# Optimization experiments

Hardware: AMD Instinct MI355X
Metric: run time of the kernel (lower is better)

The kernel has to match this reference:

```python
import jax, jax.numpy as jnp
import numpy as np

# Dims (match init_kwargs): d_model=1024, H=16 heads, hd=64, lift=2 -> Nlift=128, top-k t=32
B, T, D = 1, 2048, 1024
H, HD, LIFT, TK = 16, 64, 2, 32
N = LIFT * HD  # 128 lifted dims per head
EPS = 1e-12


def topk_sparsify(x, k):
    """ReLU then keep only the top-k values per last-dim row (rest zeroed).
    Mathematically identical to the torch COO top-k construction: the sparse
    matrix equals the dense matrix with non-top-k entries zeroed."""
    x = jax.nn.relu(x)
    vals, idx = jax.lax.top_k(x, k)              # (..., k)
    n = x.shape[-1]
    flat_idx = idx.reshape(-1, k)
    flat_vals = vals.reshape(-1, k)
    R = flat_idx.shape[0]
    out = jnp.zeros((R, n), dtype=x.dtype)
    out = out.at[jnp.arange(R)[:, None], flat_idx].set(flat_vals)
    return out.reshape(x.shape)


def setup_inputs() -> dict:
    key = jax.random.key(0)
    ks = jax.random.split(key, 6)
    x = jax.random.normal(ks[0], (B, T, D), jnp.float32)
    W_q = jax.random.normal(ks[1], (H * N, D), jnp.float32) * 0.02
    W_k = jax.random.normal(ks[2], (H * N, D), jnp.float32) * 0.02
    W_v = jax.random.normal(ks[3], (H * HD, D), jnp.float32) * 0.02
    W_o = jax.random.normal(ks[4], (D, H * HD), jnp.float32) * 0.02
    sink = jax.random.normal(ks[5], (H, HD), jnp.float32) * 0.02
    log_beta = jnp.zeros((), jnp.float32)
    return {"x": x, "W_q": W_q, "W_k": W_k, "W_v": W_v, "W_o": W_o,
            "sink": sink, "log_beta": log_beta}


def reference(x, W_q, W_k, W_v, W_o, sink, log_beta):
    # Projections (Linear with no bias: x @ W.T)
    q = (x @ W_q.T).reshape(B, T, H, N)
    k = (x @ W_k.T).reshape(B, T, H, N)
    v = (x @ W_v.T).reshape(B, T, H, HD)

    # ReLU + top-k sparsification of lifted Q/K rows
    qs = topk_sparsify(q, TK).transpose(0, 2, 1, 3)  # (B,H,T,N)
    kk = topk_sparsify(k, TK).transpose(0, 2, 1, 3)  # (B,H,T,N)

    # A = Qs @ Ks^T per (batch, head) block; spspmm only produces same-block
    # entries, so the per-head batched matmul is the exact dense equivalent.
    A = jnp.einsum('bhin,bhjn->bhij', qs, kk)        # (B,H,T,T), all >= 0

    # Causal filter: keep j <= i
    causal = jnp.tril(jnp.ones((T, T), dtype=bool))
    A = jnp.where(causal, A, jnp.zeros((), A.dtype))

    # p=1 normalization with learned sink mass beta
    denom = A.sum(-1)                                # (B,H,T)
    beta = jnp.exp(log_beta)
    denom_ws = denom + beta
    A = A / jnp.maximum(denom_ws, EPS)[..., None]

    vh = v.transpose(0, 2, 1, 3)                     # (B,H,T,HD)
    Y = jnp.einsum('bhij,bhjd->bhid', A, vh)         # (B,H,T,HD)
    Y = Y + (beta / denom_ws)[..., None] * sink[None, :, None, :]

    Y = Y.transpose(0, 2, 1, 3).reshape(B, T, H * HD)
    return Y @ W_o.T
```

## Files before the change

### kernel.cpp

```cpp
#include <hip/hip_runtime.h>

typedef __attribute__((ext_vector_type(8))) short bf8v;
typedef __attribute__((ext_vector_type(4))) float f4v;
typedef unsigned short u16;
typedef unsigned int   u32;
#define AS1 __attribute__((address_space(1)))
#define AS3 __attribute__((address_space(3)))

__device__ inline u16 f2b(float f){
  u32 u = __builtin_bit_cast(u32, f);
  u += 0x7fffu + ((u >> 16) & 1u);
  return (u16)(u >> 16);
}

__global__ __launch_bounds__(256) void conv_all(const float* __restrict__ x,  const float* __restrict__ wq,
                                                const float* __restrict__ wk, const float* __restrict__ wv,
                                                const float* __restrict__ wo,
                                                u16* xb, u16* wqb, u16* wkb, u16* wvb, u16* wob){
  int i = blockIdx.x * 256 + threadIdx.x;
  const float* src; u16* dst; int off;
  if      (i <  524288){ src = x;  dst = xb;  off = i; }
  else if (i < 1048576){ src = wq; dst = wqb; off = i -  524288; }
  else if (i < 1572864){ src = wk; dst = wkb; off = i - 1048576; }
  else if (i < 1835008){ src = wv; dst = wvb; off = i - 1572864; }
  else                 { src = wo; dst = wob; off = i - 1835008; }
  float4 v = ((const float4*)src)[off];
  uint2 r;
  r.x = (u32)f2b(v.x) | ((u32)f2b(v.y) << 16);
  r.y = (u32)f2b(v.z) | ((u32)f2b(v.w) << 16);
  ((uint2*)dst)[off] = r;
}

__device__ __forceinline__ void gemm_core(const u16* __restrict__ A, const u16* __restrict__ B,
                                          int K, int m0, int n0, u16* lds, f4v acc[4][4]){
  const int tid = threadIdx.x;
  const int l = tid & 63, w = tid >> 6;
  const int wrow = (w >> 1) * 64, wcol = (w & 1) * 64;
  #pragma unroll
  for (int a = 0; a < 4; a++)
    #pragma unroll
    for (int b = 0; b < 4; b++) acc[a][b] = (f4v)0.0f;

  const int crow = l >> 3;
  const int ksrc = ((l & 7) ^ crow) * 8;

  auto stage = [&](int k0, int buf){
    const u16* Abase = A + (size_t)m0 * K + k0;
    const u16* Bbase = B + (size_t)n0 * K + k0;
    u16* At = lds + buf * 16384;
    u16* Bt = At + 8192;
    #pragma unroll
    for (int c = 0; c < 4; c++){
      int chunk = w * 4 + c;
      int row = chunk * 8 + crow;
      __builtin_amdgcn_global_load_lds((const AS1 void*)(Abase + (size_t)row * K + ksrc),
                                       (AS3 void*)(At + chunk * 512), 16, 0, 0);
      __builtin_amdgcn_global_load_lds((const AS1 void*)(Bbase + (size_t)row * K + ksrc),
                                       (AS3 void*)(Bt + chunk * 512), 16, 0, 0);
    }
  };

  stage(0, 0);
  __syncthreads();
  int buf = 0;
  for (int k0 = 0; k0 < K; k0 += 64){
    if (k0 + 64 < K) stage(k0 + 64, buf ^ 1);
    const u16* At = lds + buf * 16384;
    const u16* Bt = At + 8192;
    #pragma unroll
    for (int kk = 0; kk < 2; kk++){
      bf8v af[4], bfr[4];
      #pragma unroll
      for (int mr = 0; mr < 4; mr++){
        int row = wrow + mr * 16 + (l & 15);
        af[mr] = *(const bf8v*)(At + row * 64 + (((kk * 32 + (l >> 4) * 8)) ^ ((row & 7) * 8)));
      }
      #pragma unroll
      for (int nc = 0; nc < 4; nc++){
        int row = wcol + nc * 16 + (l & 15);
        bfr[nc] = *(const bf8v*)(Bt + row * 64 + (((kk * 32 + (l >> 4) * 8)) ^ ((row & 7) * 8)));
      }
      #pragma unroll
      for (int mr = 0; mr < 4; mr++)
        #pragma unroll
        for (int nc = 0; nc < 4; nc++)
          acc[mr][nc] = __builtin_amdgcn_mfma_f32_16x16x32_bf16(af[mr], bfr[nc], acc[mr][nc], 0, 0, 0);
    }
    __syncthreads();
    buf ^= 1;
  }
}

__global__ __launch_bounds__(256) void qkv_gemm(const u16* __restrict__ xb,
                                                const u16* __restrict__ wqb, const u16* __restrict__ wkb,
                                                const u16* __restrict__ wvb,
                                                float* qf, float* kf, u16* vtb){
  __shared__ u16 lds[32768];
  int b = (blockIdx.x & 7) * 80 + (blockIdx.x >> 3);
  const u16* Bp; int which;
  if (b < 256)      { Bp = wqb; which = 0; }
  else if (b < 512) { Bp = wkb; which = 1; b -= 256; }
  else              { Bp = wvb; which = 2; b -= 512; }
  int sh = (which == 2) ? 3 : 4;
  int m0 = (b >> sh) * 128, n0 = (b & ((1 << sh) - 1)) * 128;

  f4v acc[4][4];
  gemm_core(xb, Bp, 1024, m0, n0, lds, acc);

  const int l = threadIdx.x & 63, w = threadIdx.x >> 6;
  const int wrow = (w >> 1) * 64, wcol = (w & 1) * 64;
  if (which < 2){
    float* C = which ? kf : qf;
    #pragma unroll
    for (int mr = 0; mr < 4; mr++)
      #pragma unroll
      for (int nc = 0; nc < 4; nc++)
        #pragma unroll
        for (int rr = 0; rr < 4; rr++){
          int row = m0 + wrow + mr * 16 + (l >> 4) * 4 + rr;
          int col = n0 + wcol + nc * 16 + (l & 15);
          C[(size_t)row * 2048 + col] = acc[mr][nc][rr];
        }
  } else {
    #pragma unroll
    for (int mr = 0; mr < 4; mr++)
      #pragma unroll
      for (int nc = 0; nc < 4; nc++){
        int gcol = n0 + wcol + nc * 16 + (l & 15);
        int t0 = m0 + wrow + mr * 16 + (l >> 4) * 4;
        uint2 pk;
        pk.x = (u32)f2b(acc[mr][nc][0]) | ((u32)f2b(acc[mr][nc][1]) << 16);
        pk.y = (u32)f2b(acc[mr][nc][2]) | ((u32)f2b(acc[mr][nc][3]) << 16);
        *(uint2*)(vtb + (size_t)gcol * 2048 + t0) = pk;
      }
  }
}

__global__ __launch_bounds__(256) void o_gemm(const u16* __restrict__ yb, const u16* __restrict__ wob,
                                              float* out){
  __shared__ u16 lds[32768];
  int b = (blockIdx.x & 7) * 16 + (blockIdx.x >> 3);
  int m0 = (b >> 3) * 128, n0 = (b & 7) * 128;
  f4v acc[4][4];
  gemm_core(yb, wob, 1024, m0, n0, lds, acc);
  const int l = threadIdx.x & 63, w = threadIdx.x >> 6;
  const int wrow = (w >> 1) * 64, wcol = (w & 1) * 64;
  #pragma unroll
  for (int mr = 0; mr < 4; mr++)
    #pragma unroll
    for (int nc = 0; nc < 4; nc++)
      #pragma unroll
      for (int rr = 0; rr < 4; rr++){
        int row = m0 + wrow + mr * 16 + (l >> 4) * 4 + rr;
        int col = n0 + wcol + nc * 16 + (l & 15);
        out[(size_t)row * 1024 + col] = acc[mr][nc][rr];
      }
}

__global__ __launch_bounds__(256) void topk2(const float* __restrict__ qf, const float* __restrict__ kf,
                                             u16* __restrict__ qsb, u16* __restrict__ ksb){
  int w = threadIdx.x >> 6, l = threadIdx.x & 63;
  int b = blockIdx.x;
  const float* src; u16* dst;
  if (b < 8192){ src = qf; dst = qsb; } else { src = kf; dst = ksb; b -= 8192; }
  int row = b * 4 + w;
  int t = row >> 4, h = row & 15;
  const float* sp = src + (size_t)t * 2048 + h * 128 + l * 2;
  float v0 = sp[0], v1 = sp[1];
  v0 = v0 > 0.f ? v0 : 0.f;
  v1 = v1 > 0.f ? v1 : 0.f;
  u32 u0 = __builtin_bit_cast(u32, v0), u1 = __builtin_bit_cast(u32, v1);
  u32 pre = 0;
  for (int bb = 30; bb >= 0; --bb){
    u32 cand = pre | (1u << bb);
    int c = __builtin_popcountll(__ballot(u0 >= cand)) + __builtin_popcountll(__ballot(u1 >= cand));
    if (c >= 32) pre = cand;
  }
  u16 o0 = (u0 >= pre) ? f2b(v0) : (u16)0;
  u16 o1 = (u1 >= pre) ? f2b(v1) : (u16)0;
  ((u32*)(dst + ((size_t)h * 2048 + t) * 128))[l] = (u32)o0 | ((u32)o1 << 16);
}

__global__ __launch_bounds__(512) void attn3(const u16* __restrict__ qs, const u16* __restrict__ ks,
                                             const u16* __restrict__ vt, const float* __restrict__ sink,
                                             const float* __restrict__ logbeta, u16* __restrict__ yout,
                                             float* __restrict__ Yp, float* __restrict__ Dp){
  __shared__ u16 Kt[2][8192];
  __shared__ u16 Vt[2][4096];
  __shared__ u16 St[8][16 * 72];
  const int tid = threadIdx.x, l = tid & 63, w = tid >> 6;
  const int b = blockIdx.x;
  const int slot = b >> 3;
  const int h = (b & 7) + 8 * (slot / 40);
  const int u = slot % 40;
  int it, chunk, nch;
  if (u < 4)       { it = u; chunk = 0; nch = 1; }
  else if (u < 12) { it = 4 + ((u - 4) >> 1);  chunk = (u - 4) & 1;  nch = 2; }
  else if (u < 24) { it = 8 + (u - 12) / 3;    chunk = (u - 12) % 3; nch = 3; }
  else             { it = 12 + ((u - 24) >> 2); chunk = (u - 24) & 3; nch = 4; }
  const int jt0 = chunk * 8;
  const int jt1 = min(jt0 + 8, 2 * it + 2);
  const int qrow0 = it * 128 + w * 16;
  const float beta = expf(logbeta[0]);

  bf8v qfr[4];
  {
    int trow = qrow0 + (l & 15);
    const u16* qrow = qs + ((size_t)h * 2048 + trow) * 128 + (l >> 4) * 8;
    #pragma unroll
    for (int kk = 0; kk < 4; kk++) qfr[kk] = *(const bf8v*)(qrow + kk * 32);
  }

  f4v accY[4];
  #pragma unroll
  for (int c = 0; c < 4; c++) accY[c] = (f4v)0.0f;
  float dsum[4] = {0.f, 0.f, 0.f, 0.f};

  const u16* kroot = ks + (size_t)h * 2048 * 128;
  const u16* vroot = vt + (size_t)h * 64 * 2048;

  auto stage = [&](int jt, int buf){
    const u16* kbase = kroot + (size_t)jt * 64 * 128;
    #pragma unroll
    for (int i = 0; i < 2; i++){
      int g = i * 512 + tid;
      int r = g >> 4, c = g & 15;
      __builtin_amdgcn_global_load_lds((const AS1 void*)(kbase + r * 128 + (c ^ (r & 7)) * 8),
                                       (AS3 void*)(&Kt[buf][(i * 512 + w * 64) * 8]), 16, 0, 0);
    }
    {
      int d = tid >> 3, c = tid & 7;
      __builtin_amdgcn_global_load_lds((const AS1 void*)(vroot + (size_t)d * 2048 + jt * 64 + (c ^ (d & 7)) * 8),
                                       (AS3 void*)(&Vt[buf][w * 512]), 16, 0, 0);
    }
  };

  stage(jt0, 0);
  __syncthreads();
  int buf = 0;
  for (int jt = jt0; jt < jt1; ++jt){
    if (jt + 1 < jt1) stage(jt + 1, buf ^ 1);

    if (jt * 64 <= qrow0 + 15){
      f4v accS[4];
      #pragma unroll
      for (int c = 0; c < 4; c++) accS[c] = (f4v)0.0f;
      __builtin_amdgcn_s_setprio(1);
      #pragma unroll
      for (int c = 0; c < 4; c++){
        int r = c * 16 + (l & 15);
        #pragma unroll
        for (int kk = 0; kk < 4; kk++){
          int ch = kk * 4 + (l >> 4);
          bf8v kfr = *(const bf8v*)(&Kt[buf][r * 128 + ((ch ^ (r & 7)) * 8)]);
          accS[c] = __builtin_amdgcn_mfma_f32_16x16x32_bf16(qfr[kk], kfr, accS[c], 0, 0, 0);
        }
      }
      __builtin_amdgcn_s_setprio(0);
      if (jt * 64 + 63 > qrow0){
        #pragma unroll
        for (int c = 0; c < 4; c++)
          #pragma unroll
          for (int rr = 0; rr < 4; rr++){
            int i = qrow0 + (l >> 4) * 4 + rr;
            int j = jt * 64 + c * 16 + (l & 15);
            if (j > i) accS[c][rr] = 0.f;
          }
      }
      #pragma unroll
      for (int c = 0; c < 4; c++)
        #pragma unroll
        for (int rr = 0; rr < 4; rr++){
          dsum[rr] += accS[c][rr];
          St[w][((l >> 4) * 4 + rr) * 72 + c * 16 + (l & 15)] = f2b(accS[c][rr]);
        }
      __builtin_amdgcn_s_setprio(1);
      #pragma unroll
      for (int k2 = 0; k2 < 2; k2++){
        bf8v afr = *(const bf8v*)(&St[w][(l & 15) * 72 + k2 * 32 + (l >> 4) * 8]);
        #pragma unroll
        for (int c = 0; c < 4; c++){
          int d = c * 16 + (l & 15);
          int ch = k2 * 4 + (l >> 4);
          bf8v vfr = *(const bf8v*)(&Vt[buf][d * 64 + ((ch ^ (d & 7)) * 8)]);
          accY[c] = __builtin_amdgcn_mfma_f32_16x16x32_bf16(afr, vfr, accY[c], 0, 0, 0);
        }
      }
      __builtin_amdgcn_s_setprio(0);
    }
    __syncthreads();
    buf ^= 1;
  }

  #pragma unroll
  for (int rr = 0; rr < 4; rr++){
    float s = dsum[rr];
    s += __shfl_xor(s, 1, 64);
    s += __shfl_xor(s, 2, 64);
    s += __shfl_xor(s, 4, 64);
    s += __shfl_xor(s, 8, 64);
    dsum[rr] = s;
  }

  if (nch == 1){
    #pragma unroll
    for (int c = 0; c < 4; c++){
      float sv = sink[h * 64 + c * 16 + (l & 15)];
      #pragma unroll
      for (int rr = 0; rr < 4; rr++){
        float den = dsum[rr] + beta;
        float inv = 1.0f / fmaxf(den, 1e-12f);
        float y = (accY[c][rr] + beta * sv) * inv;
        int row = qrow0 + (l >> 4) * 4 + rr;
        yout[(size_t)row * 1024 + h * 64 + c * 16 + (l & 15)] = f2b(y);
      }
    }
  } else {
    float* yp = Yp + ((size_t)h * 40 + u) * 8192;
    #pragma unroll
    for (int c = 0; c < 4; c++)
      #pragma unroll
      for (int rr = 0; rr < 4; rr++){
        int rowib = w * 16 + (l >> 4) * 4 + rr;
        yp[rowib * 64 + c * 16 + (l & 15)] = accY[c][rr];
      }
    if ((l & 15) == 0){
      #pragma unroll
      for (int rr = 0; rr < 4; rr++)
        Dp[((size_t)h * 40 + u) * 128 + w * 16 + (l >> 4) * 4 + rr] = dsum[rr];
    }
  }
}

__global__ __launch_bounds__(256) void attn_reduce(const float* __restrict__ Yp, const float* __restrict__ Dp,
                                                   const float* __restrict__ sink, const float* __restrict__ logbeta,
                                                   u16* __restrict__ yout){
  int blk = blockIdx.x;
  int h = blk / 12, it = 4 + blk % 12;
  int nch = it / 4 + 1;
  int u0 = (it < 8) ? 4 + (it - 4) * 2 : (it < 12) ? 12 + (it - 8) * 3 : 24 + (it - 12) * 4;
  float beta = expf(logbeta[0]);
  __shared__ float inv_s[128];
  int t = threadIdx.x;
  if (t < 128){
    float s = 0.f;
    for (int c = 0; c < nch; c++) s += Dp[((size_t)h * 40 + u0 + c) * 128 + t];
    inv_s[t] = 1.0f / fmaxf(s + beta, 1e-12f);
  }
  __syncthreads();
  const float* base = Yp + ((size_t)h * 40 + u0) * 8192;
  #pragma unroll
  for (int e = 0; e < 32; e++){
    int idx = e * 256 + t;
    float acc = 0.f;
    for (int c = 0; c < nch; c++) acc += base[c * 8192 + idx];
    int row = idx >> 6, col = idx & 63;
    float y = (acc + beta * sink[h * 64 + col]) * inv_s[row];
    yout[(size_t)(it * 128 + row) * 1024 + h * 64 + col] = f2b(y);
  }
}

extern "C" void kernel_launch(void* const* d_in, const int* in_sizes, int n_in,
                              void* d_out, int out_size, void* d_ws, size_t ws_size,
                              hipStream_t stream){
  const float* x    = (const float*)d_in[0];
  const float* Wq   = (const float*)d_in[1];
  const float* Wk   = (const float*)d_in[2];
  const float* Wv   = (const float*)d_in[3];
  const float* Wo   = (const float*)d_in[4];
  const float* sink = (const float*)d_in[5];
  const float* logb = (const float*)d_in[6];

  char* ws = (char*)d_ws;
  u16*   xb  = (u16*)(ws + 0);
  u16*   wqb = (u16*)(ws + 4194304);
  u16*   wkb = (u16*)(ws + 8388608);
  u16*   wvb = (u16*)(ws + 12582912);
  u16*   wob = (u16*)(ws + 14680064);
  float* qf  = (float*)(ws + 16777216);
  float* kf  = (float*)(ws + 33554432);
  u16*   qsb = (u16*)(ws + 50331648);
  u16*   ksb = (u16*)(ws + 58720256);
  u16*   vtb = (u16*)(ws + 67108864);
  u16*   yb  = (u16*)(ws + 71303168);
  float* Yp  = (float*)(ws + 16777216);
  float* Dp  = (float*)(ws + 37748736);

  conv_all<<<8192, 256, 0, stream>>>(x, Wq, Wk, Wv, Wo, xb, wqb, wkb, wvb, wob);
  qkv_gemm<<<640, 256, 0, stream>>>(xb, wqb, wkb, wvb, qf, kf, vtb);
  topk2<<<16384, 256, 0, stream>>>(qf, kf, qsb, ksb);
  attn3<<<640, 512, 0, stream>>>(qsb, ksb, vtb, sink, logb, yb, Yp, Dp);
  attn_reduce<<<192, 256, 0, stream>>>(Yp, Dp, sink, logb, yb);
  o_gemm<<<128, 256, 0, stream>>>(yb, wob, (float*)d_out);
}
```

Baseline: 151.5 us.

## Deepen GEMM pipeline to five-stage K32 ring and store Q/K projections as bf16

The shared GEMM core moves from a double-buffered K=64 tile loop to a five-slot ring of K=32 tiles with three stages in flight. It uses explicit vmcnt waits, a raw s_barrier and raised priority around the MFMA block, so global-to-LDS loads overlap more with compute. Separately, the QKV GEMM writes Q and K as bf16 instead of fp32, and the top-k kernel selects directly on the bf16 bits with a 15-bit radix search. This halves the projection write and read traffic. Top-k ties are now resolved at bf16 precision rather than fp32, which can change which entries are kept.

```diff
diff --git a/kernel.cpp b/kernel.cpp
--- a/kernel.cpp
+++ b/kernel.cpp
@@ -41,61 +41,71 @@
     #pragma unroll
     for (int b = 0; b < 4; b++) acc[a][b] = (f4v)0.0f;
 
-  const int crow = l >> 3;
-  const int ksrc = ((l & 7) ^ crow) * 8;
-
-  auto stage = [&](int k0, int buf){
-    const u16* Abase = A + (size_t)m0 * K + k0;
-    const u16* Bbase = B + (size_t)n0 * K + k0;
-    u16* At = lds + buf * 16384;
-    u16* Bt = At + 8192;
-    #pragma unroll
-    for (int c = 0; c < 4; c++){
-      int chunk = w * 4 + c;
-      int row = chunk * 8 + crow;
-      __builtin_amdgcn_global_load_lds((const AS1 void*)(Abase + (size_t)row * K + ksrc),
-                                       (AS3 void*)(At + chunk * 512), 16, 0, 0);
-      __builtin_amdgcn_global_load_lds((const AS1 void*)(Bbase + (size_t)row * K + ksrc),
-                                       (AS3 void*)(Bt + chunk * 512), 16, 0, 0);
-    }
+  const int c0 = w * 64 + l;
+  const int c1 = c0 + 256;
+  const int r0 = c0 >> 2, s0e = ((c0 & 3) ^ ((r0 >> 1) & 3)) * 8;
+  const int r1 = c1 >> 2, s1e = ((c1 & 3) ^ ((r1 >> 1) & 3)) * 8;
+
+  const u16* Aroot = A + (size_t)m0 * K;
+  const u16* Broot = B + (size_t)n0 * K;
+
+  auto stage = [&](int k0, int bb){
+    const u16* Ab = Aroot + k0;
+    const u16* Bb = Broot + k0;
+    __builtin_amdgcn_global_load_lds((const AS1 void*)(Ab + (size_t)r0 * K + s0e),
+                                     (AS3 void*)(lds + bb + w * 512), 16, 0, 0);
+    __builtin_amdgcn_global_load_lds((const AS1 void*)(Ab + (size_t)r1 * K + s1e),
+                                     (AS3 void*)(lds + bb + 2048 + w * 512), 16, 0, 0);
+    __builtin_amdgcn_global_load_lds((const AS1 void*)(Bb + (size_t)r0 * K + s0e),
+                                     (AS3 void*)(lds + bb + 4096 + w * 512), 16, 0, 0);
+    __builtin_amdgcn_global_load_lds((const AS1 void*)(Bb + (size_t)r1 * K + s1e),
+                                     (AS3 void*)(lds + bb + 6144 + w * 512), 16, 0, 0);
   };
 
+  const int nst = K >> 5;
   stage(0, 0);
-  __syncthreads();
-  int buf = 0;
-  for (int k0 = 0; k0 < K; k0 += 64){
-    if (k0 + 64 < K) stage(k0 + 64, buf ^ 1);
-    const u16* At = lds + buf * 16384;
-    const u16* Bt = At + 8192;
-    #pragma unroll
-    for (int kk = 0; kk < 2; kk++){
-      bf8v af[4], bfr[4];
-      #pragma unroll
-      for (int mr = 0; mr < 4; mr++){
-        int row = wrow + mr * 16 + (l & 15);
-        af[mr] = *(const bf8v*)(At + row * 64 + (((kk * 32 + (l >> 4) * 8)) ^ ((row & 7) * 8)));
-      }
-      #pragma unroll
-      for (int nc = 0; nc < 4; nc++){
-        int row = wcol + nc * 16 + (l & 15);
-        bfr[nc] = *(const bf8v*)(Bt + row * 64 + (((kk * 32 + (l >> 4) * 8)) ^ ((row & 7) * 8)));
-      }
-      #pragma unroll
-      for (int mr = 0; mr < 4; mr++)
-        #pragma unroll
-        for (int nc = 0; nc < 4; nc++)
-          acc[mr][nc] = __builtin_amdgcn_mfma_f32_16x16x32_bf16(af[mr], bfr[nc], acc[mr][nc], 0, 0, 0);
-    }
-    __syncthreads();
-    buf ^= 1;
+  stage(32, 8192);
+  stage(64, 16384);
+
+  const int kb = l >> 4;
+  for (int i = 0; i < nst; ++i){
+    int k3 = (i + 3) << 5;
+    if (k3 < K) stage(k3, ((i + 3) % 5) * 8192);
+    if      (i <  nst - 3) asm volatile("s_waitcnt vmcnt(12)" ::: "memory");
+    else if (i == nst - 3) asm volatile("s_waitcnt vmcnt(8)"  ::: "memory");
+    else if (i == nst - 2) asm volatile("s_waitcnt vmcnt(4)"  ::: "memory");
+    else                   asm volatile("s_waitcnt vmcnt(0)"  ::: "memory");
+    __builtin_amdgcn_sched_barrier(0);
+    __builtin_amdgcn_s_barrier();
+
+    const u16* At = lds + (i % 5) * 8192;
+    const u16* Bt = At + 4096;
+    bf8v af[4], bfr[4];
+    #pragma unroll
+    for (int mr = 0; mr < 4; mr++){
+      int row = wrow + mr * 16 + (l & 15);
+      af[mr] = *(const bf8v*)(At + row * 32 + ((kb ^ ((row >> 1) & 3)) * 8));
+    }
+    #pragma unroll
+    for (int nc = 0; nc < 4; nc++){
+      int row = wcol + nc * 16 + (l & 15);
+      bfr[nc] = *(const bf8v*)(Bt + row * 32 + ((kb ^ ((row >> 1) & 3)) * 8));
+    }
+    __builtin_amdgcn_s_setprio(1);
+    #pragma unroll
+    for (int mr = 0; mr < 4; mr++)
+      #pragma unroll
+      for (int nc = 0; nc < 4; nc++)
+        acc[mr][nc] = __builtin_amdgcn_mfma_f32_16x16x32_bf16(af[mr], bfr[nc], acc[mr][nc], 0, 0, 0);
+    __builtin_amdgcn_s_setprio(0);
   }
 }
 
 __global__ __launch_bounds__(256) void qkv_gemm(const u16* __restrict__ xb,
                                                 const u16* __restrict__ wqb, const u16* __restrict__ wkb,
                                                 const u16* __restrict__ wvb,
-                                                float* qf, float* kf, u16* vtb){
-  __shared__ u16 lds[32768];
+                                                u16* qf, u16* kf, u16* vtb){
+  __shared__ u16 lds[40960];
   int b = (blockIdx.x & 7) * 80 + (blockIdx.x >> 3);
   const u16* Bp; int which;
   if (b < 256)      { Bp = wqb; which = 0; }
@@ -110,7 +120,7 @@
   const int l = threadIdx.x & 63, w = threadIdx.x >> 6;
   const int wrow = (w >> 1) * 64, wcol = (w & 1) * 64;
   if (which < 2){
-    float* C = which ? kf : qf;
+    u16* C = which ? kf : qf;
     #pragma unroll
     for (int mr = 0; mr < 4; mr++)
       #pragma unroll
@@ -119,7 +129,7 @@
         for (int rr = 0; rr < 4; rr++){
           int row = m0 + wrow + mr * 16 + (l >> 4) * 4 + rr;
           int col = n0 + wcol + nc * 16 + (l & 15);
-          C[(size_t)row * 2048 + col] = acc[mr][nc][rr];
+          C[(size_t)row * 2048 + col] = f2b(acc[mr][nc][rr]);
         }
   } else {
     #pragma unroll
@@ -138,7 +148,7 @@
 
 __global__ __launch_bounds__(256) void o_gemm(const u16* __restrict__ yb, const u16* __restrict__ wob,
                                               float* out){
-  __shared__ u16 lds[32768];
+  __shared__ u16 lds[40960];
   int b = (blockIdx.x & 7) * 16 + (blockIdx.x >> 3);
   int m0 = (b >> 3) * 128, n0 = (b & 7) * 128;
   f4v acc[4][4];
@@ -157,28 +167,27 @@
       }
 }
 
-__global__ __launch_bounds__(256) void topk2(const float* __restrict__ qf, const float* __restrict__ kf,
+__global__ __launch_bounds__(256) void topk2(const u16* __restrict__ qf, const u16* __restrict__ kf,
                                              u16* __restrict__ qsb, u16* __restrict__ ksb){
   int w = threadIdx.x >> 6, l = threadIdx.x & 63;
   int b = blockIdx.x;
-  const float* src; u16* dst;
+  const u16* src; u16* dst;
   if (b < 8192){ src = qf; dst = qsb; } else { src = kf; dst = ksb; b -= 8192; }
   int row = b * 4 + w;
   int t = row >> 4, h = row & 15;
-  const float* sp = src + (size_t)t * 2048 + h * 128 + l * 2;
-  float v0 = sp[0], v1 = sp[1];
-  v0 = v0 > 0.f ? v0 : 0.f;
-  v1 = v1 > 0.f ? v1 : 0.f;
-  u32 u0 = __builtin_bit_cast(u32, v0), u1 = __builtin_bit_cast(u32, v1);
+  u32 pair = ((const u32*)(src + (size_t)t * 2048 + h * 128))[l];
+  u32 u0 = pair & 0xFFFFu, u1 = pair >> 16;
+  if (u0 & 0x8000u) u0 = 0;
+  if (u1 & 0x8000u) u1 = 0;
   u32 pre = 0;
-  for (int bb = 30; bb >= 0; --bb){
+  for (int bb = 14; bb >= 0; --bb){
     u32 cand = pre | (1u << bb);
     int c = __builtin_popcountll(__ballot(u0 >= cand)) + __builtin_popcountll(__ballot(u1 >= cand));
     if (c >= 32) pre = cand;
   }
-  u16 o0 = (u0 >= pre) ? f2b(v0) : (u16)0;
-  u16 o1 = (u1 >= pre) ? f2b(v1) : (u16)0;
-  ((u32*)(dst + ((size_t)h * 2048 + t) * 128))[l] = (u32)o0 | ((u32)o1 << 16);
+  u32 o0 = (u0 >= pre) ? u0 : 0u;
+  u32 o1 = (u1 >= pre) ? u1 : 0u;
+  ((u32*)(dst + ((size_t)h * 2048 + t) * 128))[l] = o0 | (o1 << 16);
 }
 
 __global__ __launch_bounds__(512) void attn3(const u16* __restrict__ qs, const u16* __restrict__ ks,
@@ -377,8 +386,8 @@
   u16*   wkb = (u16*)(ws + 8388608);
   u16*   wvb = (u16*)(ws + 12582912);
   u16*   wob = (u16*)(ws + 14680064);
-  float* qf  = (float*)(ws + 16777216);
-  float* kf  = (float*)(ws + 33554432);
+  u16*   qf  = (u16*)(ws + 16777216);
+  u16*   kf  = (u16*)(ws + 33554432);
   u16*   qsb = (u16*)(ws + 50331648);
   u16*   ksb = (u16*)(ws + 58720256);
   u16*   vtb = (u16*)(ws + 67108864);
```

Result: faster. 145.1 us (-4.2%).

## Fuse ReLU+top-k into QKV GEMM epilogue, shrink O-GEMM tiles, rebalance attention chunks

Applied to the files above, without the earlier changes.

The ReLU and top-k selection move into the Q/K projection GEMM epilogue. The bf16 tile is staged in LDS and a 15-bit radix search runs on bf16 bits, which removes the fp32 Q/K round trip through global memory and the separate topk2 launch. Top-k is now selected on bf16-rounded values, so ties after rounding can change which entries are kept. The output GEMM switches to 128x64 tiles so 256 blocks launch instead of 128, improving CU occupancy. Attention key-tile chunks are split evenly across chunks instead of in fixed runs of 8.

```diff
diff --git a/kernel.cpp b/kernel.cpp
--- a/kernel.cpp
+++ b/kernel.cpp
@@ -31,32 +31,49 @@
   ((uint2*)dst)[off] = r;
 }
 
+template<int NFR>
 __device__ __forceinline__ void gemm_core(const u16* __restrict__ A, const u16* __restrict__ B,
-                                          int K, int m0, int n0, u16* lds, f4v acc[4][4]){
+                                          int K, int m0, int n0, u16* lds, f4v (&acc)[4][NFR]){
   const int tid = threadIdx.x;
   const int l = tid & 63, w = tid >> 6;
-  const int wrow = (w >> 1) * 64, wcol = (w & 1) * 64;
+  const int wrow = (w >> 1) * 64, wcol = (w & 1) * (NFR * 16);
+  constexpr int SB = 8192 + NFR * 2048;
   #pragma unroll
   for (int a = 0; a < 4; a++)
     #pragma unroll
-    for (int b = 0; b < 4; b++) acc[a][b] = (f4v)0.0f;
+    for (int b = 0; b < NFR; b++) acc[a][b] = (f4v)0.0f;
 
   const int crow = l >> 3;
   const int ksrc = ((l & 7) ^ crow) * 8;
 
   auto stage = [&](int k0, int buf){
-    const u16* Abase = A + (size_t)m0 * K + k0;
-    const u16* Bbase = B + (size_t)n0 * K + k0;
-    u16* At = lds + buf * 16384;
+    const u16* Ab = A + (size_t)m0 * K + k0;
+    const u16* Bb = B + (size_t)n0 * K + k0;
+    u16* At = lds + buf * SB;
     u16* Bt = At + 8192;
     #pragma unroll
     for (int c = 0; c < 4; c++){
       int chunk = w * 4 + c;
       int row = chunk * 8 + crow;
-      __builtin_amdgcn_global_load_lds((const AS1 void*)(Abase + (size_t)row * K + ksrc),
+      __builtin_amdgcn_global_load_lds((const AS1 void*)(Ab + (size_t)row * K + ksrc),
                                        (AS3 void*)(At + chunk * 512), 16, 0, 0);
-      __builtin_amdgcn_global_load_lds((const AS1 void*)(Bbase + (size_t)row * K + ksrc),
-                                       (AS3 void*)(Bt + chunk * 512), 16, 0, 0);
+    }
+    if constexpr (NFR == 4){
+      #pragma unroll
+      for (int c = 0; c < 4; c++){
+        int chunk = w * 4 + c;
+        int row = chunk * 8 + crow;
+        __builtin_amdgcn_global_load_lds((const AS1 void*)(Bb + (size_t)row * K + ksrc),
+                                         (AS3 void*)(Bt + chunk * 512), 16, 0, 0);
+      }
+    } else {
+      #pragma unroll
+      for (int c = 0; c < 2; c++){
+        int chunk = w * 2 + c;
+        int row = chunk * 8 + crow;
+        __builtin_amdgcn_global_load_lds((const AS1 void*)(Bb + (size_t)row * K + ksrc),
+                                         (AS3 void*)(Bt + chunk * 512), 16, 0, 0);
+      }
     }
   };
 
@@ -65,25 +82,25 @@
   int buf = 0;
   for (int k0 = 0; k0 < K; k0 += 64){
     if (k0 + 64 < K) stage(k0 + 64, buf ^ 1);
-    const u16* At = lds + buf * 16384;
+    const u16* At = lds + buf * SB;
     const u16* Bt = At + 8192;
     #pragma unroll
     for (int kk = 0; kk < 2; kk++){
-      bf8v af[4], bfr[4];
+      bf8v af[4], bfr[NFR];
       #pragma unroll
       for (int mr = 0; mr < 4; mr++){
         int row = wrow + mr * 16 + (l & 15);
         af[mr] = *(const bf8v*)(At + row * 64 + (((kk * 32 + (l >> 4) * 8)) ^ ((row & 7) * 8)));
       }
       #pragma unroll
-      for (int nc = 0; nc < 4; nc++){
+      for (int nc = 0; nc < NFR; nc++){
         int row = wcol + nc * 16 + (l & 15);
         bfr[nc] = *(const bf8v*)(Bt + row * 64 + (((kk * 32 + (l >> 4) * 8)) ^ ((row & 7) * 8)));
       }
       #pragma unroll
       for (int mr = 0; mr < 4; mr++)
         #pragma unroll
-        for (int nc = 0; nc < 4; nc++)
+        for (int nc = 0; nc < NFR; nc++)
           acc[mr][nc] = __builtin_amdgcn_mfma_f32_16x16x32_bf16(af[mr], bfr[nc], acc[mr][nc], 0, 0, 0);
     }
     __syncthreads();
@@ -94,7 +111,7 @@
 __global__ __launch_bounds__(256) void qkv_gemm(const u16* __restrict__ xb,
                                                 const u16* __restrict__ wqb, const u16* __restrict__ wkb,
                                                 const u16* __restrict__ wvb,
-                                                float* qf, float* kf, u16* vtb){
+                                                u16* qsb, u16* ksb, u16* vtb){
   __shared__ u16 lds[32768];
   int b = (blockIdx.x & 7) * 80 + (blockIdx.x >> 3);
   const u16* Bp; int which;
@@ -105,22 +122,40 @@
   int m0 = (b >> sh) * 128, n0 = (b & ((1 << sh) - 1)) * 128;
 
   f4v acc[4][4];
-  gemm_core(xb, Bp, 1024, m0, n0, lds, acc);
+  gemm_core<4>(xb, Bp, 1024, m0, n0, lds, acc);
 
   const int l = threadIdx.x & 63, w = threadIdx.x >> 6;
   const int wrow = (w >> 1) * 64, wcol = (w & 1) * 64;
   if (which < 2){
-    float* C = which ? kf : qf;
+    u16* Sc = lds;
     #pragma unroll
     for (int mr = 0; mr < 4; mr++)
       #pragma unroll
       for (int nc = 0; nc < 4; nc++)
         #pragma unroll
         for (int rr = 0; rr < 4; rr++){
-          int row = m0 + wrow + mr * 16 + (l >> 4) * 4 + rr;
-          int col = n0 + wcol + nc * 16 + (l & 15);
-          C[(size_t)row * 2048 + col] = acc[mr][nc][rr];
+          int row = wrow + mr * 16 + (l >> 4) * 4 + rr;
+          int col = wcol + nc * 16 + (l & 15);
+          float v = acc[mr][nc][rr];
+          Sc[row * 132 + col] = (v > 0.f) ? f2b(v) : (u16)0;
         }
+    __syncthreads();
+    u16* dst = which ? ksb : qsb;
+    const int h = n0 >> 7;
+    for (int r2 = 0; r2 < 32; ++r2){
+      int r = w * 32 + r2;
+      u32 pair = *(const u32*)(Sc + r * 132 + l * 2);
+      u32 u0 = pair & 0xFFFFu, u1 = pair >> 16;
+      u32 pre = 0;
+      for (int bb = 14; bb >= 0; --bb){
+        u32 cand = pre | (1u << bb);
+        int c = __builtin_popcountll(__ballot(u0 >= cand)) + __builtin_popcountll(__ballot(u1 >= cand));
+        if (c >= 32) pre = cand;
+      }
+      u32 o0 = (u0 >= pre) ? u0 : 0u;
+      u32 o1 = (u1 >= pre) ? u1 : 0u;
+      ((u32*)(dst + ((size_t)h * 2048 + m0 + r) * 128))[l] = o0 | (o1 << 16);
+    }
   } else {
     #pragma unroll
     for (int mr = 0; mr < 4; mr++)
@@ -138,47 +173,23 @@
 
 __global__ __launch_bounds__(256) void o_gemm(const u16* __restrict__ yb, const u16* __restrict__ wob,
                                               float* out){
-  __shared__ u16 lds[32768];
-  int b = (blockIdx.x & 7) * 16 + (blockIdx.x >> 3);
-  int m0 = (b >> 3) * 128, n0 = (b & 7) * 128;
-  f4v acc[4][4];
-  gemm_core(yb, wob, 1024, m0, n0, lds, acc);
+  __shared__ u16 lds[24576];
+  int b = (blockIdx.x & 7) * 32 + (blockIdx.x >> 3);
+  int m0 = (b >> 4) * 128, n0 = (b & 15) * 64;
+  f4v acc[4][2];
+  gemm_core<2>(yb, wob, 1024, m0, n0, lds, acc);
   const int l = threadIdx.x & 63, w = threadIdx.x >> 6;
-  const int wrow = (w >> 1) * 64, wcol = (w & 1) * 64;
+  const int wrow = (w >> 1) * 64, wcol = (w & 1) * 32;
   #pragma unroll
   for (int mr = 0; mr < 4; mr++)
     #pragma unroll
-    for (int nc = 0; nc < 4; nc++)
+    for (int nc = 0; nc < 2; nc++)
       #pragma unroll
       for (int rr = 0; rr < 4; rr++){
         int row = m0 + wrow + mr * 16 + (l >> 4) * 4 + rr;
         int col = n0 + wcol + nc * 16 + (l & 15);
         out[(size_t)row * 1024 + col] = acc[mr][nc][rr];
       }
-}
-
-__global__ __launch_bounds__(256) void topk2(const float* __restrict__ qf, const float* __restrict__ kf,
-                                             u16* __restrict__ qsb, u16* __restrict__ ksb){
-  int w = threadIdx.x >> 6, l = threadIdx.x & 63;
-  int b = blockIdx.x;
-  const float* src; u16* dst;
-  if (b < 8192){ src = qf; dst = qsb; } else { src = kf; dst = ksb; b -= 8192; }
-  int row = b * 4 + w;
-  int t = row >> 4, h = row & 15;
-  const float* sp = src + (size_t)t * 2048 + h * 128 + l * 2;
-  float v0 = sp[0], v1 = sp[1];
-  v0 = v0 > 0.f ? v0 : 0.f;
-  v1 = v1 > 0.f ? v1 : 0.f;
-  u32 u0 = __builtin_bit_cast(u32, v0), u1 = __builtin_bit_cast(u32, v1);
-  u32 pre = 0;
-  for (int bb = 30; bb >= 0; --bb){
-    u32 cand = pre | (1u << bb);
-    int c = __builtin_popcountll(__ballot(u0 >= cand)) + __builtin_popcountll(__ballot(u1 >= cand));
-    if (c >= 32) pre = cand;
-  }
-  u16 o0 = (u0 >= pre) ? f2b(v0) : (u16)0;
-  u16 o1 = (u1 >= pre) ? f2b(v1) : (u16)0;
-  ((u32*)(dst + ((size_t)h * 2048 + t) * 128))[l] = (u32)o0 | ((u32)o1 << 16);
 }
 
 __global__ __launch_bounds__(512) void attn3(const u16* __restrict__ qs, const u16* __restrict__ ks,
@@ -198,8 +209,9 @@
   else if (u < 12) { it = 4 + ((u - 4) >> 1);  chunk = (u - 4) & 1;  nch = 2; }
   else if (u < 24) { it = 8 + (u - 12) / 3;    chunk = (u - 12) % 3; nch = 3; }
   else             { it = 12 + ((u - 24) >> 2); chunk = (u - 24) & 3; nch = 4; }
-  const int jt0 = chunk * 8;
-  const int jt1 = min(jt0 + 8, 2 * it + 2);
+  const int tiles = 2 * it + 2;
+  const int jt0 = (tiles * chunk) / nch;
+  const int jt1 = (tiles * (chunk + 1)) / nch;
   const int qrow0 = it * 128 + w * 16;
   const float beta = expf(logbeta[0]);
 
@@ -377,19 +389,16 @@
   u16*   wkb = (u16*)(ws + 8388608);
   u16*   wvb = (u16*)(ws + 12582912);
   u16*   wob = (u16*)(ws + 14680064);
-  float* qf  = (float*)(ws + 16777216);
-  float* kf  = (float*)(ws + 33554432);
+  float* Yp  = (float*)(ws + 16777216);
+  float* Dp  = (float*)(ws + 37748736);
   u16*   qsb = (u16*)(ws + 50331648);
   u16*   ksb = (u16*)(ws + 58720256);
   u16*   vtb = (u16*)(ws + 67108864);
   u16*   yb  = (u16*)(ws + 71303168);
-  float* Yp  = (float*)(ws + 16777216);
-  float* Dp  = (float*)(ws + 37748736);
 
   conv_all<<<8192, 256, 0, stream>>>(x, Wq, Wk, Wv, Wo, xb, wqb, wkb, wvb, wob);
-  qkv_gemm<<<640, 256, 0, stream>>>(xb, wqb, wkb, wvb, qf, kf, vtb);
-  topk2<<<16384, 256, 0, stream>>>(qf, kf, qsb, ksb);
+  qkv_gemm<<<640, 256, 0, stream>>>(xb, wqb, wkb, wvb, qsb, ksb, vtb);
   attn3<<<640, 512, 0, stream>>>(qsb, ksb, vtb, sink, logb, yb, Yp, Dp);
   attn_reduce<<<192, 256, 0, stream>>>(Yp, Dp, sink, logb, yb);
-  o_gemm<<<128, 256, 0, stream>>>(yb, wob, (float*)d_out);
-}
+  o_gemm<<<256, 256, 0, stream>>>(yb, wob, (float*)d_out);
+}
```

Measured after the change: 149.6 us. About the same (-1.2%).
